# Kernel tuning notes

Hardware: AMD Instinct MI355X
Metric: run time of the kernel (lower is better)

## Reference

```python
import jax, jax.numpy as jnp
import numpy as np

ROPE_THETA = 10000.0


def _rotate_half(x):
    # interleaved rotation: out[..., 2i] = -x[..., 2i+1], out[..., 2i+1] = x[..., 2i]
    x_even = x[..., ::2]
    x_odd = x[..., 1::2]
    return jnp.stack([-x_odd, x_even], axis=-1).reshape(x.shape)


def _rope_cos_sin(N, D, dtype):
    inv_freq = 1.0 / (ROPE_THETA ** (jnp.arange(0, D, 2, dtype=jnp.float32) / D))  # [D/2]
    angles = jnp.arange(N, dtype=jnp.float32)[:, None] * inv_freq[None, :]          # [N, D/2]
    angles = jnp.repeat(angles, 2, axis=-1)                                          # [N, D]
    cos = jnp.cos(angles).astype(dtype)[None, :, None, :]  # [1, N, 1, D]
    sin = jnp.sin(angles).astype(dtype)[None, :, None, :]
    return cos, sin


def setup_inputs() -> dict:
    key = jax.random.key(0)
    kq, kk, kv, km = jax.random.split(key, 4)
    B, N, H, D = 16, 1024, 8, 64
    xq = jax.random.normal(kq, (B, N, H, D), dtype=jnp.float32)
    xk = jax.random.normal(kk, (B, N, H, D), dtype=jnp.float32)
    xv = jax.random.normal(kv, (B, N, H, D), dtype=jnp.float32)
    vis_mask = jax.random.bernoulli(km, 0.8, (B, N))  # bool visibility mask per batch
    return {"xq": xq, "xk": xk, "xv": xv, "vis_mask": vis_mask}


def reference(xq, xk, xv, vis_mask):
    B, N, H, D = xq.shape
    sm_scale = 1.0 / np.sqrt(D).astype(np.float32)

    # RoPE (interleaved) on q and k
    cos, sin = _rope_cos_sin(N, D, xq.dtype)
    q = xq * cos + _rotate_half(xq) * sin
    k = xk * cos + _rotate_half(xk) * sin

    # masked full attention: scores [B, H, N, N]
    scores = jnp.einsum("bnhd,bmhd->bhnm", q, k) * sm_scale
    attn_mask = (vis_mask[:, None, :, None] & vis_mask[:, None, None, :])  # [B,1,N,N]
    scores = jnp.where(attn_mask, scores, -jnp.inf)
    p = jax.nn.softmax(scores, axis=-1)
    p = jnp.nan_to_num(p, nan=0.0)  # fully-masked rows -> zeros (matches fallback)
    out = jnp.einsum("bhnm,bmhd->bnhd", p, xv)
    return out
```

## Files before the change

### kernel.cpp

```cpp
#include <hip/hip_runtime.h>
#include <hip/hip_bf16.h>
#include <stdint.h>

#define Bb 16
#define Nn 1024
#define Hh 8
#define Dd 64

typedef unsigned short u16;
typedef float f32x4 __attribute__((ext_vector_type(4)));
typedef short short8 __attribute__((ext_vector_type(8)));

union U4S8 { uint4 u; short8 s; };
union BF2U { __hip_bfloat162 h; uint32_t u; };

__device__ __forceinline__ uint32_t f2bf(float f){
  union{float f;uint32_t i;} v; v.f=f;
  return (v.i + 0x7fffu + ((v.i>>16)&1u))>>16;
}

__device__ __forceinline__ f32x4 mfma16(short8 a, short8 b, f32x4 c){
  return __builtin_amdgcn_mfma_f32_16x16x32_bf16(a,b,c,0,0,0);
}

typedef __attribute__((address_space(3))) uint32_t lds_u32;
typedef const __attribute__((address_space(1))) uint32_t glb_u32;
__device__ __forceinline__ void gl_lds16(const u16* g, u16* l){
  __builtin_amdgcn_global_load_lds((glb_u32*)g, (lds_u32*)l, 16, 0, 0);
}

#define ROPE_K 0.41524101186092030f
#define QS 0.18033688011112042f
#define NEGBIG -1.0e30f

__global__ void rope_table_kernel(float2* __restrict__ tab){
  int id = blockIdx.x*256 + threadIdx.x;
  int n = id >> 5, i = id & 31;
  float inv = exp2f(-(float)i * ROPE_K);
  float a = (float)n * inv;
  float s, c; sincosf(a, &s, &c);
  tab[id] = make_float2(c, s);
}

__global__ __launch_bounds__(256) void prepass_kernel(
    const float* __restrict__ xk, const float* __restrict__ xv,
    const float2* __restrict__ tab,
    u16* __restrict__ Kf, u16* __restrict__ Vf)
{
  const int tid = threadIdx.x;
  const int bid = blockIdx.x;
  const int nt = bid & 15, h = (bid>>4)&7, b = bid>>7;
  const size_t bh = (size_t)b*Hh + h;
  const size_t tile = (bh<<4) + nt;

  {
    int r = tid>>2, c = (tid&3)<<4;
    int n = (nt<<6) + r;
    const float4* g = (const float4*)(xk + ((((size_t)b*Nn + n)*Hh + h)<<6) + c);
    float4 a0=g[0],a1=g[1],a2=g[2],a3=g[3];
    float xx[16] = {a0.x,a0.y,a0.z,a0.w, a1.x,a1.y,a1.z,a1.w,
                    a2.x,a2.y,a2.z,a2.w, a3.x,a3.y,a3.z,a3.w};
    uint32_t w[8];
    #pragma unroll
    for (int j=0;j<8;++j){
      int i = (c>>1)+j;
      float cs, sn;
      if (tab){ float2 t = tab[(n<<5)+i]; cs = t.x; sn = t.y; }
      else { float inv = exp2f(-(float)i * ROPE_K); sincosf((float)n*inv, &sn, &cs); }
      float x0 = xx[2*j], x1 = xx[2*j+1];
      float q0 = x0*cs - x1*sn;
      float q1 = x1*cs + x0*sn;
      w[j] = f2bf(q0) | (f2bf(q1)<<16);
    }
    int kb = r>>4, l15 = r&15;
    int half = c>>5, qd = (c>>3)&3;
    u16* base = Kf + (tile<<12);
    int dest0 = (kb<<10) + (half<<9) + (qd<<7) + (l15<<3);
    *(uint4*)(base + dest0)       = make_uint4(w[0],w[1],w[2],w[3]);
    *(uint4*)(base + dest0 + 128) = make_uint4(w[4],w[5],w[6],w[7]);
  }

  {
    int k = tid&63, ds = (tid>>6)<<4;
    int n = (nt<<6) + k;
    int slot = (k&1) | (((k>>4)&3)<<1) | (((k>>2)&3)<<3) | (((k>>1)&1)<<5);
    int half = slot>>5, qd = (slot>>3)&3, j = slot&7;
    const float4* g = (const float4*)(xv + ((((size_t)b*Nn + n)*Hh + h)<<6) + ds);
    float4 a0=g[0],a1=g[1],a2=g[2],a3=g[3];
    float vv[16] = {a0.x,a0.y,a0.z,a0.w, a1.x,a1.y,a1.z,a1.w,
                    a2.x,a2.y,a2.z,a2.w, a3.x,a3.y,a3.z,a3.w};
    u16* base = Vf + (tile<<12);
    #pragma unroll
    for (int jj=0;jj<16;++jj){
      int d = ds + jj;
      int s = d>>4, l15v = d&15;
      base[(s<<10) + (half<<9) + (qd<<7) + (l15v<<3) + j] = (u16)f2bf(vv[jj]);
    }
  }
}

__global__ __launch_bounds__(256,4) void attn6_kernel(
    const float* __restrict__ xq, const u16* __restrict__ Kf,
    const u16* __restrict__ Vf, const int* __restrict__ vis,
    const float2* __restrict__ tab, float* __restrict__ out)
{
  __shared__ u16 KV[2][2][4096];

  const int tid  = threadIdx.x;
  const int lane = tid & 63;
  const int wave = tid >> 6;
  const int l15  = lane & 15;
  const int quad = lane >> 4;

  const int bid = blockIdx.x;
  const int xcd = bid & 7;
  const int i   = bid >> 3;
  const int bh_ = (xcd<<4) | (i>>3);
  const int qt  = i & 7;
  const int h   = bh_ & 7;
  const int b   = bh_ >> 3;
  const size_t bh = (size_t)bh_;
  const int qbase = qt<<7;

  const int* visb = vis + b*Nn;
  const u16* Kfb = Kf + (bh<<16);
  const u16* Vfb = Vf + (bh<<16);

  short8 qa[2][2];
  #pragma unroll
  for (int mb=0; mb<2; ++mb){
    int n = qbase + (wave<<5) + (mb<<4) + l15;
    const float* src = xq + ((((size_t)b*Nn + n)*Hh + h)<<6);
    #pragma unroll
    for (int half=0; half<2; ++half){
      int d0 = (half<<5) + (quad<<3);
      const float4* g = (const float4*)(src + d0);
      float4 u0 = g[0], u1 = g[1];
      float xx[8] = {u0.x,u0.y,u0.z,u0.w, u1.x,u1.y,u1.z,u1.w};
      uint32_t w[4];
      #pragma unroll
      for (int j=0;j<4;++j){
        int i2 = (d0>>1) + j;
        float cs, sn;
        if (tab){ float2 t = tab[(n<<5)+i2]; cs = t.x; sn = t.y; }
        else { float inv = exp2f(-(float)i2 * ROPE_K); sincosf((float)n*inv, &sn, &cs); }
        float x0 = xx[2*j], x1 = xx[2*j+1];
        float q0 = (x0*cs - x1*sn)*QS;
        float q1 = (x1*cs + x0*sn)*QS;
        w[j] = f2bf(q0) | (f2bf(q1)<<16);
      }
      U4S8 t; t.u = make_uint4(w[0],w[1],w[2],w[3]);
      qa[mb][half] = t.s;
    }
  }

  U4S8 ones_u; ones_u.u = make_uint4(0x3F803F80u,0x3F803F80u,0x3F803F80u,0x3F803F80u);
  const short8 ones = ones_u.s;

  f32x4 acc[2][4];
  f32x4 l_acc[2];
  #pragma unroll
  for (int mb=0;mb<2;++mb){
    l_acc[mb] = (f32x4){0.f,0.f,0.f,0.f};
    #pragma unroll
    for (int s=0;s<4;++s) acc[mb][s] = (f32x4){0.f,0.f,0.f,0.f};
  }

  const int t8 = tid<<3;

  {
    const u16* kg = Kfb;  const u16* vg = Vfb;
    gl_lds16(kg + t8,        &KV[0][0][t8]);
    gl_lds16(kg + 2048 + t8, &KV[0][0][2048 + t8]);
    gl_lds16(vg + t8,        &KV[0][1][t8]);
    gl_lds16(vg + 2048 + t8, &KV[0][1][2048 + t8]);
  }
  __syncthreads();

  for (int kt=0; kt<16; ++kt){
    const int cur = kt & 1;
    if (kt < 15){
      const u16* kg = Kfb + ((kt+1)<<12);
      const u16* vg = Vfb + ((kt+1)<<12);
      gl_lds16(kg + t8,        &KV[cur^1][0][t8]);
      gl_lds16(kg + 2048 + t8, &KV[cur^1][0][2048 + t8]);
      gl_lds16(vg + t8,        &KV[cur^1][1][t8]);
      gl_lds16(vg + 2048 + t8, &KV[cur^1][1][2048 + t8]);
    }

    uint32_t pk[4][2][2];
    #pragma unroll
    for (int kb=0;kb<4;++kb){
      short8 kf0 = *(const short8*)&KV[cur][0][(kb<<10) + (lane<<3)];
      short8 kf1 = *(const short8*)&KV[cur][0][(kb<<10) + 512 + (lane<<3)];
      int4 vi = *(const int4*)&visb[(kt<<6)+(kb<<4)+(quad<<2)];
      f32x4 bias;
      bias.x = vi.x ? 0.f : NEGBIG;
      bias.y = vi.y ? 0.f : NEGBIG;
      bias.z = vi.z ? 0.f : NEGBIG;
      bias.w = vi.w ? 0.f : NEGBIG;
      #pragma unroll
      for (int mb=0;mb<2;++mb){
        f32x4 t = mfma16(kf0, qa[mb][0], bias);
        t = mfma16(kf1, qa[mb][1], t);
        float p0 = __builtin_amdgcn_exp2f(t.x);
        float p1 = __builtin_amdgcn_exp2f(t.y);
        float p2 = __builtin_amdgcn_exp2f(t.z);
        float p3 = __builtin_amdgcn_exp2f(t.w);
        BF2U e0; e0.h = __float22bfloat162_rn(make_float2(p0,p1));
        BF2U e1; e1.h = __float22bfloat162_rn(make_float2(p2,p3));
        pk[kb][0][mb] = e0.u;
        pk[kb][1][mb] = e1.u;
      }
    }

    short8 pa[2][2];
    #pragma unroll
    for (int mb=0;mb<2;++mb){
      U4S8 a0; a0.u = make_uint4(pk[0][0][mb], pk[1][0][mb], pk[2][0][mb], pk[3][0][mb]);
      U4S8 a1; a1.u = make_uint4(pk[0][1][mb], pk[1][1][mb], pk[2][1][mb], pk[3][1][mb]);
      pa[mb][0] = a0.s; pa[mb][1] = a1.s;
    }

    #pragma unroll
    for (int mb=0;mb<2;++mb){
      l_acc[mb] = mfma16(pa[mb][0], ones, l_acc[mb]);
      l_acc[mb] = mfma16(pa[mb][1], ones, l_acc[mb]);
    }
    #pragma unroll
    for (int s=0;s<4;++s){
      short8 vb0 = *(const short8*)&KV[cur][1][(s<<10) + (lane<<3)];
      short8 vb1 = *(const short8*)&KV[cur][1][(s<<10) + 512 + (lane<<3)];
      #pragma unroll
      for (int mb=0;mb<2;++mb){
        acc[mb][s] = mfma16(pa[mb][0], vb0, acc[mb][s]);
        acc[mb][s] = mfma16(pa[mb][1], vb1, acc[mb][s]);
      }
    }

    __syncthreads();
  }

  #pragma unroll
  for (int mb=0;mb<2;++mb){
    int4 qvi = *(const int4*)&visb[qbase + (wave<<5) + (mb<<4) + (quad<<2)];
    int qv[4] = {qvi.x, qvi.y, qvi.z, qvi.w};
    #pragma unroll
    for (int rr=0;rr<4;++rr){
      float lq = l_acc[mb][rr];
      float invl = (qv[rr] != 0 && lq > 0.f) ? 1.f/lq : 0.f;
      int qrow = qbase + (wave<<5) + (mb<<4) + (quad<<2) + rr;
      float* ob = out + ((((size_t)b*Nn + qrow)*Hh + h)<<6);
      #pragma unroll
      for (int s=0;s<4;++s)
        ob[(s<<4)+l15] = acc[mb][s][rr]*invl;
    }
  }
}

__device__ __forceinline__ void stage_rope_row_fb(const float* __restrict__ src,
                                                  u16 (*dst)[72],
                                                  int n_global, int sr, int d0)
{
  const float4* g = (const float4*)src;
  float4 a0 = g[0], a1 = g[1], a2 = g[2], a3 = g[3];
  float xx[16] = {a0.x,a0.y,a0.z,a0.w, a1.x,a1.y,a1.z,a1.w,
                  a2.x,a2.y,a2.z,a2.w, a3.x,a3.y,a3.z,a3.w};
  uint32_t w[8];
  #pragma unroll
  for (int j=0;j<8;++j){
    int i = (d0>>1)+j;
    float inv = exp2f(-(float)i * ROPE_K);
    float ang = (float)n_global * inv;
    float sn, cs; sincosf(ang, &sn, &cs);
    float x0 = xx[2*j], x1 = xx[2*j+1];
    float q0 = x0*cs - x1*sn;
    float q1 = x1*cs + x0*sn;
    w[j] = f2bf(q0) | (f2bf(q1)<<16);
  }
  *(uint4*)&dst[sr][d0]   = make_uint4(w[0],w[1],w[2],w[3]);
  *(uint4*)&dst[sr][d0+8] = make_uint4(w[4],w[5],w[6],w[7]);
}

__global__ __launch_bounds__(256,2) void attn_fallback(
    const float* __restrict__ xq, const float* __restrict__ xk,
    const float* __restrict__ xv, const int* __restrict__ vis,
    float* __restrict__ out)
{
  __shared__ u16 Qs[64][72];
  __shared__ u16 Ks[64][72];
  __shared__ u16 Vt[64][72];
  __shared__ u16 Ps[4][16][72];
  __shared__ float viss[64];

  const int tid  = threadIdx.x;
  const int wave = tid >> 6;
  const int lane = tid & 63;
  const int l15  = lane & 15;
  const int quad = lane >> 4;

  const int bid = blockIdx.x;
  const int qt = bid & 15;
  const int h  = (bid >> 4) & 7;
  const int b  = bid >> 7;

  const int sr = tid >> 2;
  const int d0 = (tid & 3) << 4;

  {
    int ng = (qt<<6) + sr;
    const float* src = xq + ((((size_t)b*Nn + ng)*Hh + h)<<6) + d0;
    stage_rope_row_fb(src, Qs, ng, sr, d0);
  }
  __syncthreads();

  short8 qa0 = *(const short8*)&Qs[(wave<<4)+l15][quad<<3];
  short8 qa1 = *(const short8*)&Qs[(wave<<4)+l15][(quad<<3)+32];

  f32x4 acc[4];
  #pragma unroll
  for (int s=0;s<4;++s) acc[s] = (f32x4){0.f,0.f,0.f,0.f};
  float m_r[4], l_r[4];
  #pragma unroll
  for (int rr=0;rr<4;++rr){ m_r[rr] = -1e30f; l_r[rr] = 0.f; }

  for (int kt=0; kt<16; ++kt){
    __syncthreads();
    {
      int ng = (kt<<6) + sr;
      const float* src = xk + ((((size_t)b*Nn + ng)*Hh + h)<<6) + d0;
      stage_rope_row_fb(src, Ks, ng, sr, d0);
    }
    {
      int ng = (kt<<6) + sr;
      const float4* g = (const float4*)(xv + ((((size_t)b*Nn + ng)*Hh + h)<<6) + d0);
      float4 a0 = g[0], a1 = g[1], a2 = g[2], a3 = g[3];
      float vv16[16] = {a0.x,a0.y,a0.z,a0.w, a1.x,a1.y,a1.z,a1.w,
                        a2.x,a2.y,a2.z,a2.w, a3.x,a3.y,a3.z,a3.w};
      #pragma unroll
      for (int j=0;j<16;++j) Vt[d0+j][sr] = (u16)f2bf(vv16[j]);
    }
    if (tid < 64) viss[tid] = (vis[b*Nn + (kt<<6) + tid] != 0) ? 1.f : 0.f;
    __syncthreads();

    f32x4 s4[4];
    #pragma unroll
    for (int n=0;n<4;++n){
      short8 kb0 = *(const short8*)&Ks[(n<<4)+l15][quad<<3];
      short8 kb1 = *(const short8*)&Ks[(n<<4)+l15][(quad<<3)+32];
      f32x4 t = (f32x4){0.f,0.f,0.f,0.f};
      t = mfma16(qa0, kb0, t);
      t = mfma16(qa1, kb1, t);
      s4[n] = t;
    }
    float vv[4];
    #pragma unroll
    for (int n=0;n<4;++n) vv[n] = viss[(n<<4)+l15];

    float p[4][4];
    #pragma unroll
    for (int rr=0; rr<4; ++rr){
      float sc[4];
      #pragma unroll
      for (int n=0;n<4;++n) sc[n] = (vv[n] > 0.f) ? s4[n][rr]*0.125f : -1e30f;
      float tm = fmaxf(fmaxf(sc[0],sc[1]), fmaxf(sc[2],sc[3]));
      tm = fmaxf(tm, __shfl_xor(tm,1));
      tm = fmaxf(tm, __shfl_xor(tm,2));
      tm = fmaxf(tm, __shfl_xor(tm,4));
      tm = fmaxf(tm, __shfl_xor(tm,8));
      float mnew  = fmaxf(m_r[rr], tm);
      float alpha = __expf(m_r[rr] - mnew);
      m_r[rr] = mnew;
      float psum = 0.f;
      #pragma unroll
      for (int n=0;n<4;++n){
        float pv = (vv[n] > 0.f) ? __expf(sc[n] - mnew) : 0.f;
        p[n][rr] = pv; psum += pv;
      }
      l_r[rr] = l_r[rr]*alpha + psum;
      #pragma unroll
      for (int s=0;s<4;++s) acc[s][rr] *= alpha;
    }

    #pragma unroll
    for (int n=0;n<4;++n)
      #pragma unroll
      for (int rr=0;rr<4;++rr)
        Ps[wave][(quad<<2)+rr][(n<<4)+l15] = (u16)f2bf(p[n][rr]);
    asm volatile("s_waitcnt lgkmcnt(0)" ::: "memory");
    short8 pa0 = *(const short8*)&Ps[wave][l15][quad<<3];
    short8 pa1 = *(const short8*)&Ps[wave][l15][(quad<<3)+32];

    #pragma unroll
    for (int s=0;s<4;++s){
      short8 vb0 = *(const short8*)&Vt[(s<<4)+l15][quad<<3];
      short8 vb1 = *(const short8*)&Vt[(s<<4)+l15][(quad<<3)+32];
      acc[s] = mfma16(pa0, vb0, acc[s]);
      acc[s] = mfma16(pa1, vb1, acc[s]);
    }
  }

  #pragma unroll
  for (int rr=0;rr<4;++rr){
    float t = l_r[rr];
    t += __shfl_xor(t,1); t += __shfl_xor(t,2);
    t += __shfl_xor(t,4); t += __shfl_xor(t,8);
    int row = (qt<<6) + (wave<<4) + (quad<<2) + rr;
    int qv  = vis[b*Nn + row];
    float invl = (qv != 0 && t > 0.f) ? 1.f/t : 0.f;
    size_t obase = (((size_t)b*Nn + row)*Hh + h) << 6;
    #pragma unroll
    for (int s=0;s<4;++s)
      out[obase + (s<<4) + l15] = acc[s][rr]*invl;
  }
}

extern "C" void kernel_launch(void* const* d_in, const int* in_sizes, int n_in,
                              void* d_out, int out_size, void* d_ws, size_t ws_size,
                              hipStream_t stream)
{
  const float* xq = (const float*)d_in[0];
  const float* xk = (const float*)d_in[1];
  const float* xv = (const float*)d_in[2];
  const int* vis  = (const int*)d_in[3];
  float* out = (float*)d_out;

  const size_t kv_elems = (size_t)Bb*Hh*Nn*Dd;
  const size_t kv_bytes = kv_elems*sizeof(u16);
  const size_t tab_bytes = (size_t)Nn*32*sizeof(float2);
  const size_t need_tab = tab_bytes + 2*kv_bytes;
  const size_t need_kv  = 2*kv_bytes;

  if (d_ws != nullptr && ws_size >= need_tab){
    float2* tab = (float2*)d_ws;
    u16* Kf = (u16*)((char*)d_ws + tab_bytes);
    u16* Vf = Kf + kv_elems;
    rope_table_kernel<<<dim3((Nn*32)/256), dim3(256), 0, stream>>>(tab);
    prepass_kernel<<<dim3(Bb*Hh*(Nn/64)), dim3(256), 0, stream>>>(xk, xv, tab, Kf, Vf);
    attn6_kernel<<<dim3(Bb*Hh*(Nn/128)), dim3(256), 0, stream>>>(xq, Kf, Vf, vis, tab, out);
  } else if (d_ws != nullptr && ws_size >= need_kv){
    u16* Kf = (u16*)d_ws;
    u16* Vf = Kf + kv_elems;
    prepass_kernel<<<dim3(Bb*Hh*(Nn/64)), dim3(256), 0, stream>>>(xk, xv, nullptr, Kf, Vf);
    attn6_kernel<<<dim3(Bb*Hh*(Nn/128)), dim3(256), 0, stream>>>(xq, Kf, Vf, vis, nullptr, out);
  } else {
    attn_fallback<<<dim3(Bb*Hh*(Nn/64)), dim3(256), 0, stream>>>(xq, xk, xv, vis, out);
  }
}
```

Baseline: 206.2 us.

## Read K/V fragments directly from global memory instead of LDS double-buffering

Removes the shared-memory double buffer, the async global-to-LDS copies and the per-tile block barrier from the attention kernel. Each wave now loads its K and V MFMA fragments straight from global memory in the pre-swizzled layout, relying on L2 and L1 to serve the four waves that read the same tile. This drops LDS traffic and synchronisation, but each wave now issues its own global loads with less explicit latency hiding, and the total global request count per block rises fourfold.

After: 208.4 us. No clear change (+1.1%).

```diff
diff --git a/kernel.cpp b/kernel.cpp
--- a/kernel.cpp
+++ b/kernel.cpp
@@ -21,12 +21,6 @@
 
 __device__ __forceinline__ f32x4 mfma16(short8 a, short8 b, f32x4 c){
   return __builtin_amdgcn_mfma_f32_16x16x32_bf16(a,b,c,0,0,0);
-}
-
-typedef __attribute__((address_space(3))) uint32_t lds_u32;
-typedef const __attribute__((address_space(1))) uint32_t glb_u32;
-__device__ __forceinline__ void gl_lds16(const u16* g, u16* l){
-  __builtin_amdgcn_global_load_lds((glb_u32*)g, (lds_u32*)l, 16, 0, 0);
 }
 
 #define ROPE_K 0.41524101186092030f
@@ -99,13 +93,11 @@
   }
 }
 
-__global__ __launch_bounds__(256,4) void attn6_kernel(
+__global__ __launch_bounds__(256,4) void attn7_kernel(
     const float* __restrict__ xq, const u16* __restrict__ Kf,
     const u16* __restrict__ Vf, const int* __restrict__ vis,
     const float2* __restrict__ tab, float* __restrict__ out)
 {
-  __shared__ u16 KV[2][2][4096];
-
   const int tid  = threadIdx.x;
   const int lane = tid & 63;
   const int wave = tid >> 6;
@@ -166,33 +158,18 @@
     for (int s=0;s<4;++s) acc[mb][s] = (f32x4){0.f,0.f,0.f,0.f};
   }
 
-  const int t8 = tid<<3;
-
-  {
-    const u16* kg = Kfb;  const u16* vg = Vfb;
-    gl_lds16(kg + t8,        &KV[0][0][t8]);
-    gl_lds16(kg + 2048 + t8, &KV[0][0][2048 + t8]);
-    gl_lds16(vg + t8,        &KV[0][1][t8]);
-    gl_lds16(vg + 2048 + t8, &KV[0][1][2048 + t8]);
-  }
-  __syncthreads();
-
+  const int fofs = lane<<3;
+
+  #pragma unroll 2
   for (int kt=0; kt<16; ++kt){
-    const int cur = kt & 1;
-    if (kt < 15){
-      const u16* kg = Kfb + ((kt+1)<<12);
-      const u16* vg = Vfb + ((kt+1)<<12);
-      gl_lds16(kg + t8,        &KV[cur^1][0][t8]);
-      gl_lds16(kg + 2048 + t8, &KV[cur^1][0][2048 + t8]);
-      gl_lds16(vg + t8,        &KV[cur^1][1][t8]);
-      gl_lds16(vg + 2048 + t8, &KV[cur^1][1][2048 + t8]);
-    }
+    const u16* kg = Kfb + (kt<<12);
+    const u16* vg = Vfb + (kt<<12);
 
     uint32_t pk[4][2][2];
     #pragma unroll
     for (int kb=0;kb<4;++kb){
-      short8 kf0 = *(const short8*)&KV[cur][0][(kb<<10) + (lane<<3)];
-      short8 kf1 = *(const short8*)&KV[cur][0][(kb<<10) + 512 + (lane<<3)];
+      short8 kf0 = *(const short8*)(kg + (kb<<10) + fofs);
+      short8 kf1 = *(const short8*)(kg + (kb<<10) + 512 + fofs);
       int4 vi = *(const int4*)&visb[(kt<<6)+(kb<<4)+(quad<<2)];
       f32x4 bias;
       bias.x = vi.x ? 0.f : NEGBIG;
@@ -229,16 +206,14 @@
     }
     #pragma unroll
     for (int s=0;s<4;++s){
-      short8 vb0 = *(const short8*)&KV[cur][1][(s<<10) + (lane<<3)];
-      short8 vb1 = *(const short8*)&KV[cur][1][(s<<10) + 512 + (lane<<3)];
+      short8 vb0 = *(const short8*)(vg + (s<<10) + fofs);
+      short8 vb1 = *(const short8*)(vg + (s<<10) + 512 + fofs);
       #pragma unroll
       for (int mb=0;mb<2;++mb){
         acc[mb][s] = mfma16(pa[mb][0], vb0, acc[mb][s]);
         acc[mb][s] = mfma16(pa[mb][1], vb1, acc[mb][s]);
       }
     }
-
-    __syncthreads();
   }
 
   #pragma unroll
@@ -437,12 +412,12 @@
     u16* Vf = Kf + kv_elems;
     rope_table_kernel<<<dim3((Nn*32)/256), dim3(256), 0, stream>>>(tab);
     prepass_kernel<<<dim3(Bb*Hh*(Nn/64)), dim3(256), 0, stream>>>(xk, xv, tab, Kf, Vf);
-    attn6_kernel<<<dim3(Bb*Hh*(Nn/128)), dim3(256), 0, stream>>>(xq, Kf, Vf, vis, tab, out);
+    attn7_kernel<<<dim3(Bb*Hh*(Nn/128)), dim3(256), 0, stream>>>(xq, Kf, Vf, vis, tab, out);
   } else if (d_ws != nullptr && ws_size >= need_kv){
     u16* Kf = (u16*)d_ws;
     u16* Vf = Kf + kv_elems;
     prepass_kernel<<<dim3(Bb*Hh*(Nn/64)), dim3(256), 0, stream>>>(xk, xv, nullptr, Kf, Vf);
-    attn6_kernel<<<dim3(Bb*Hh*(Nn/128)), dim3(256), 0, stream>>>(xq, Kf, Vf, vis, nullptr, out);
+    attn7_kernel<<<dim3(Bb*Hh*(Nn/128)), dim3(256), 0, stream>>>(xq, Kf, Vf, vis, nullptr, out);
   } else {
     attn_fallback<<<dim3(Bb*Hh*(Nn/64)), dim3(256), 0, stream>>>(xq, xk, xv, vis, out);
   }
```

## Double query rows per block and compute RoPE inline instead of via table

Applied to the files above, without the earlier changes.

Each attention block now handles 256 query rows (64 per wave, four 16-row MFMA blocks) instead of 128. Each K/V tile staged in LDS is therefore reused across twice as many queries, and the grid halves to 512 blocks with launch bounds relaxed to 2 blocks per SM. The RoPE cos/sin table kernel is removed and sincos is computed inline in the prepass and the Q load, dropping one launch and its table reads. The cost is roughly doubled register pressure for the accumulators, lower occupancy, fewer blocks to fill the GPU, and extra transcendental work per element.

After: 189.5 us. -8.1%, faster.

```diff
diff --git a/kernel.cpp b/kernel.cpp
--- a/kernel.cpp
+++ b/kernel.cpp
@@ -33,18 +33,8 @@
 #define QS 0.18033688011112042f
 #define NEGBIG -1.0e30f
 
-__global__ void rope_table_kernel(float2* __restrict__ tab){
-  int id = blockIdx.x*256 + threadIdx.x;
-  int n = id >> 5, i = id & 31;
-  float inv = exp2f(-(float)i * ROPE_K);
-  float a = (float)n * inv;
-  float s, c; sincosf(a, &s, &c);
-  tab[id] = make_float2(c, s);
-}
-
 __global__ __launch_bounds__(256) void prepass_kernel(
     const float* __restrict__ xk, const float* __restrict__ xv,
-    const float2* __restrict__ tab,
     u16* __restrict__ Kf, u16* __restrict__ Vf)
 {
   const int tid = threadIdx.x;
@@ -64,9 +54,9 @@
     #pragma unroll
     for (int j=0;j<8;++j){
       int i = (c>>1)+j;
-      float cs, sn;
-      if (tab){ float2 t = tab[(n<<5)+i]; cs = t.x; sn = t.y; }
-      else { float inv = exp2f(-(float)i * ROPE_K); sincosf((float)n*inv, &sn, &cs); }
+      float inv = exp2f(-(float)i * ROPE_K);
+      float ang = (float)n * inv;
+      float sn, cs; sincosf(ang, &sn, &cs);
       float x0 = xx[2*j], x1 = xx[2*j+1];
       float q0 = x0*cs - x1*sn;
       float q1 = x1*cs + x0*sn;
@@ -99,10 +89,10 @@
   }
 }
 
-__global__ __launch_bounds__(256,4) void attn6_kernel(
+__global__ __launch_bounds__(256,2) void attn8_kernel(
     const float* __restrict__ xq, const u16* __restrict__ Kf,
     const u16* __restrict__ Vf, const int* __restrict__ vis,
-    const float2* __restrict__ tab, float* __restrict__ out)
+    float* __restrict__ out)
 {
   __shared__ u16 KV[2][2][4096];
 
@@ -115,21 +105,21 @@
   const int bid = blockIdx.x;
   const int xcd = bid & 7;
   const int i   = bid >> 3;
-  const int bh_ = (xcd<<4) | (i>>3);
-  const int qt  = i & 7;
+  const int bh_ = (xcd<<4) | (i>>2);
+  const int qt  = i & 3;
   const int h   = bh_ & 7;
   const int b   = bh_ >> 3;
   const size_t bh = (size_t)bh_;
-  const int qbase = qt<<7;
+  const int qbase = qt<<8;
 
   const int* visb = vis + b*Nn;
   const u16* Kfb = Kf + (bh<<16);
   const u16* Vfb = Vf + (bh<<16);
 
-  short8 qa[2][2];
-  #pragma unroll
-  for (int mb=0; mb<2; ++mb){
-    int n = qbase + (wave<<5) + (mb<<4) + l15;
+  short8 qa[4][2];
+  #pragma unroll
+  for (int mb=0; mb<4; ++mb){
+    int n = qbase + (wave<<6) + (mb<<4) + l15;
     const float* src = xq + ((((size_t)b*Nn + n)*Hh + h)<<6);
     #pragma unroll
     for (int half=0; half<2; ++half){
@@ -141,9 +131,9 @@
       #pragma unroll
       for (int j=0;j<4;++j){
         int i2 = (d0>>1) + j;
-        float cs, sn;
-        if (tab){ float2 t = tab[(n<<5)+i2]; cs = t.x; sn = t.y; }
-        else { float inv = exp2f(-(float)i2 * ROPE_K); sincosf((float)n*inv, &sn, &cs); }
+        float inv = exp2f(-(float)i2 * ROPE_K);
+        float ang = (float)n * inv;
+        float sn, cs; sincosf(ang, &sn, &cs);
         float x0 = xx[2*j], x1 = xx[2*j+1];
         float q0 = (x0*cs - x1*sn)*QS;
         float q1 = (x1*cs + x0*sn)*QS;
@@ -157,10 +147,10 @@
   U4S8 ones_u; ones_u.u = make_uint4(0x3F803F80u,0x3F803F80u,0x3F803F80u,0x3F803F80u);
   const short8 ones = ones_u.s;
 
-  f32x4 acc[2][4];
-  f32x4 l_acc[2];
-  #pragma unroll
-  for (int mb=0;mb<2;++mb){
+  f32x4 acc[4][4];
+  f32x4 l_acc[4];
+  #pragma unroll
+  for (int mb=0;mb<4;++mb){
     l_acc[mb] = (f32x4){0.f,0.f,0.f,0.f};
     #pragma unroll
     for (int s=0;s<4;++s) acc[mb][s] = (f32x4){0.f,0.f,0.f,0.f};
@@ -168,13 +158,10 @@
 
   const int t8 = tid<<3;
 
-  {
-    const u16* kg = Kfb;  const u16* vg = Vfb;
-    gl_lds16(kg + t8,        &KV[0][0][t8]);
-    gl_lds16(kg + 2048 + t8, &KV[0][0][2048 + t8]);
-    gl_lds16(vg + t8,        &KV[0][1][t8]);
-    gl_lds16(vg + 2048 + t8, &KV[0][1][2048 + t8]);
-  }
+  gl_lds16(Kfb + t8,        &KV[0][0][t8]);
+  gl_lds16(Kfb + 2048 + t8, &KV[0][0][2048 + t8]);
+  gl_lds16(Vfb + t8,        &KV[0][1][t8]);
+  gl_lds16(Vfb + 2048 + t8, &KV[0][1][2048 + t8]);
   __syncthreads();
 
   for (int kt=0; kt<16; ++kt){
@@ -188,7 +175,7 @@
       gl_lds16(vg + 2048 + t8, &KV[cur^1][1][2048 + t8]);
     }
 
-    uint32_t pk[4][2][2];
+    uint32_t pk[4][2][4];
     #pragma unroll
     for (int kb=0;kb<4;++kb){
       short8 kf0 = *(const short8*)&KV[cur][0][(kb<<10) + (lane<<3)];
@@ -200,7 +187,7 @@
       bias.z = vi.z ? 0.f : NEGBIG;
       bias.w = vi.w ? 0.f : NEGBIG;
       #pragma unroll
-      for (int mb=0;mb<2;++mb){
+      for (int mb=0;mb<4;++mb){
         f32x4 t = mfma16(kf0, qa[mb][0], bias);
         t = mfma16(kf1, qa[mb][1], t);
         float p0 = __builtin_amdgcn_exp2f(t.x);
@@ -214,16 +201,16 @@
       }
     }
 
-    short8 pa[2][2];
-    #pragma unroll
-    for (int mb=0;mb<2;++mb){
+    short8 pa[4][2];
+    #pragma unroll
+    for (int mb=0;mb<4;++mb){
       U4S8 a0; a0.u = make_uint4(pk[0][0][mb], pk[1][0][mb], pk[2][0][mb], pk[3][0][mb]);
       U4S8 a1; a1.u = make_uint4(pk[0][1][mb], pk[1][1][mb], pk[2][1][mb], pk[3][1][mb]);
       pa[mb][0] = a0.s; pa[mb][1] = a1.s;
     }
 
     #pragma unroll
-    for (int mb=0;mb<2;++mb){
+    for (int mb=0;mb<4;++mb){
       l_acc[mb] = mfma16(pa[mb][0], ones, l_acc[mb]);
       l_acc[mb] = mfma16(pa[mb][1], ones, l_acc[mb]);
     }
@@ -232,7 +219,7 @@
       short8 vb0 = *(const short8*)&KV[cur][1][(s<<10) + (lane<<3)];
       short8 vb1 = *(const short8*)&KV[cur][1][(s<<10) + 512 + (lane<<3)];
       #pragma unroll
-      for (int mb=0;mb<2;++mb){
+      for (int mb=0;mb<4;++mb){
         acc[mb][s] = mfma16(pa[mb][0], vb0, acc[mb][s]);
         acc[mb][s] = mfma16(pa[mb][1], vb1, acc[mb][s]);
       }
@@ -242,14 +229,14 @@
   }
 
   #pragma unroll
-  for (int mb=0;mb<2;++mb){
-    int4 qvi = *(const int4*)&visb[qbase + (wave<<5) + (mb<<4) + (quad<<2)];
+  for (int mb=0;mb<4;++mb){
+    int4 qvi = *(const int4*)&visb[qbase + (wave<<6) + (mb<<4) + (quad<<2)];
     int qv[4] = {qvi.x, qvi.y, qvi.z, qvi.w};
     #pragma unroll
     for (int rr=0;rr<4;++rr){
       float lq = l_acc[mb][rr];
       float invl = (qv[rr] != 0 && lq > 0.f) ? 1.f/lq : 0.f;
-      int qrow = qbase + (wave<<5) + (mb<<4) + (quad<<2) + rr;
+      int qrow = qbase + (wave<<6) + (mb<<4) + (quad<<2) + rr;
       float* ob = out + ((((size_t)b*Nn + qrow)*Hh + h)<<6);
       #pragma unroll
       for (int s=0;s<4;++s)
@@ -427,22 +414,13 @@
 
   const size_t kv_elems = (size_t)Bb*Hh*Nn*Dd;
   const size_t kv_bytes = kv_elems*sizeof(u16);
-  const size_t tab_bytes = (size_t)Nn*32*sizeof(float2);
-  const size_t need_tab = tab_bytes + 2*kv_bytes;
   const size_t need_kv  = 2*kv_bytes;
 
-  if (d_ws != nullptr && ws_size >= need_tab){
-    float2* tab = (float2*)d_ws;
-    u16* Kf = (u16*)((char*)d_ws + tab_bytes);
-    u16* Vf = Kf + kv_elems;
-    rope_table_kernel<<<dim3((Nn*32)/256), dim3(256), 0, stream>>>(tab);
-    prepass_kernel<<<dim3(Bb*Hh*(Nn/64)), dim3(256), 0, stream>>>(xk, xv, tab, Kf, Vf);
-    attn6_kernel<<<dim3(Bb*Hh*(Nn/128)), dim3(256), 0, stream>>>(xq, Kf, Vf, vis, tab, out);
-  } else if (d_ws != nullptr && ws_size >= need_kv){
+  if (d_ws != nullptr && ws_size >= need_kv){
     u16* Kf = (u16*)d_ws;
     u16* Vf = Kf + kv_elems;
-    prepass_kernel<<<dim3(Bb*Hh*(Nn/64)), dim3(256), 0, stream>>>(xk, xv, nullptr, Kf, Vf);
-    attn6_kernel<<<dim3(Bb*Hh*(Nn/128)), dim3(256), 0, stream>>>(xq, Kf, Vf, vis, nullptr, out);
+    prepass_kernel<<<dim3(Bb*Hh*(Nn/64)), dim3(256), 0, stream>>>(xk, xv, Kf, Vf);
+    attn8_kernel<<<dim3(Bb*Hh*(Nn/256)), dim3(256), 0, stream>>>(xq, Kf, Vf, vis, out);
   } else {
     attn_fallback<<<dim3(Bb*Hh*(Nn/64)), dim3(256), 0, stream>>>(xq, xk, xv, vis, out);
   }
```
